# Kernel tuning notes

Measured on AMD Instinct MI355X. Metric: run time of the kernel, lower is better.

## Reference

```python
import jax, jax.numpy as jnp
import numpy as np

N_NODES = 100_000
E_OFF = 1_000_000
HID = 32
GF = 8
NF = 8
N_LAYERS = 3


def _mlp(h, W1, b1, W2, b2):
    # Linear -> ReLU -> Linear (matches MLP([in, hidden, out]))
    return jax.nn.relu(h @ W1 + b1) @ W2 + b2


def _seg_mean(v, idx, n):
    s = jax.ops.segment_sum(v, idx, num_segments=n)
    c = jax.ops.segment_sum(jnp.ones((v.shape[0], 1), v.dtype), idx, num_segments=n)
    return s / jnp.maximum(c, 1.0)


def _graphnet(x, row, col, eattr2, g, p):
    # GraphNet with global block: edge MLP -> mean-aggregate to nodes -> node MLP -> global MLP
    eW1, eb1, eW2, eb2, nW1, nb1, nW2, nb2, gW1, gb1, gW2, gb2 = p
    n, e = x.shape[0], row.shape[0]
    gE = jnp.broadcast_to(g, (e, g.shape[1]))
    e_emb = _mlp(jnp.concatenate([gE, x[row], x[col], eattr2], axis=1), eW1, eb1, eW2, eb2)
    agg = _seg_mean(e_emb, row, n)
    gN = jnp.broadcast_to(g, (n, g.shape[1]))
    n_emb = _mlp(jnp.concatenate([gN, x, agg], axis=1), nW1, nb1, nW2, nb2)
    g_new = _mlp(jnp.concatenate([n_emb.mean(0, keepdims=True), e_emb.mean(0, keepdims=True), g], axis=1),
                 gW1, gb1, gW2, gb2)
    return e_emb, n_emb, g_new


def setup_inputs() -> dict:
    key = jax.random.key(0)
    ks = jax.random.split(key, 24)
    a = jax.random.randint(ks[0], (E_OFF,), 0, N_NODES)
    b = jax.random.randint(ks[1], (E_OFF,), 0, N_NODES)
    d = jnp.arange(N_NODES)
    l_ei = jnp.stack([jnp.concatenate([jnp.maximum(a, b), d]),
                      jnp.concatenate([jnp.minimum(a, b), d])])  # lower triangular + diag
    c = jax.random.randint(ks[2], (E_OFF,), 0, N_NODES)
    e = jax.random.randint(ks[3], (E_OFF,), 0, N_NODES)
    u_ei = jnp.stack([jnp.concatenate([jnp.minimum(c, e), d]),
                      jnp.concatenate([jnp.maximum(c, e), d])])  # upper triangular + diag
    E = E_OFF + N_NODES
    x = jax.random.normal(ks[4], (N_NODES, NF), dtype=jnp.float32)
    l_attr = jax.random.normal(ks[5], (E, 1), dtype=jnp.float32)
    u_attr = jax.random.normal(ks[6], (E, 1), dtype=jnp.float32)

    def w(k, shape):
        return (jax.random.normal(k, shape, dtype=jnp.float32) / np.sqrt(shape[-2])).astype(jnp.float32)

    e_in = GF + 2 * NF + 1 + 1  # 26 (edge attr padded to 2: skip col, zeros where absent)
    n_in = GF + 1 + NF          # 17
    g_in = NF + 1 + GF          # 17
    return {
        'x': x, 'l_edge_index': l_ei, 'u_edge_index': u_ei,
        'l_edge_attr': l_attr, 'u_edge_attr': u_attr,
        'eW1': w(ks[7], (2, N_LAYERS, e_in, HID)), 'eb1': 0.01 * jax.random.normal(ks[8], (2, N_LAYERS, HID)),
        'eW2': w(ks[9], (2, N_LAYERS, HID, 1)), 'eb2': 0.01 * jax.random.normal(ks[10], (2, N_LAYERS, 1)),
        'nW1': w(ks[11], (2, N_LAYERS, n_in, HID)), 'nb1': 0.01 * jax.random.normal(ks[12], (2, N_LAYERS, HID)),
        'nW2': w(ks[13], (2, N_LAYERS, HID, NF)), 'nb2': 0.01 * jax.random.normal(ks[14], (2, N_LAYERS, NF)),
        'gW1': w(ks[15], (2, N_LAYERS, g_in, HID)), 'gb1': 0.01 * jax.random.normal(ks[16], (2, N_LAYERS, HID)),
        'gW2': w(ks[17], (2, N_LAYERS, HID, GF)), 'gb2': 0.01 * jax.random.normal(ks[18], (2, N_LAYERS, GF)),
    }


def reference(x, l_edge_index, u_edge_index, l_edge_attr, u_edge_attr,
              eW1, eb1, eW2, eb2, nW1, nb1, nW2, nb2, gW1, gb1, gW2, gb2):
    params = (eW1, eb1, eW2, eb2, nW1, nb1, nW2, nb2, gW1, gb1, gW2, gb2)
    lr, lc = l_edge_index[0], l_edge_index[1]
    ur, uc = u_edge_index[0], u_edge_index[1]
    g = jnp.zeros((1, GF), x.dtype)
    l_e, u_e = l_edge_attr, u_edge_attr
    l_a = l_edge_attr  # skip-connection edge features (original matrix values)
    zl, zu = jnp.zeros_like(l_edge_attr), jnp.zeros_like(u_edge_attr)
    for i in range(N_LAYERS):
        p1 = tuple(w[0, i] for w in params)
        p2 = tuple(w[1, i] for w in params)
        l_in = jnp.concatenate([l_e, l_a if i != 0 else zl], axis=1)  # zeros col == no skip (block 0)
        l_e, l_n, g = _graphnet(x, lr, lc, l_in, g, p1)
        u_in = jnp.concatenate([u_e, zu], axis=1)  # l2 never has skip; padded zeros col
        u_e, u_n, g = _graphnet(l_n, ur, uc, u_in, g, p2)
        # NOTE: node embeddings are NOT carried across MP blocks in the original
    l_vals = jnp.where(lr == lc, jnp.exp(l_e[:, 0]), l_e[:, 0])
    u_vals = jnp.where(ur == uc, jnp.exp(u_e[:, 0]), u_e[:, 0])
    return jnp.concatenate([l_vals, u_vals])
```

## Files before the change

### kernel.cpp

```cpp
#include <hip/hip_runtime.h>


typedef unsigned int u32;

#define NB_SHIFT 9
#define NB_SIZE 512
#define RSTRIDE 1104

__device__ __forceinline__ float wave_sum(float v) {
#pragma unroll
    for (int off = 32; off > 0; off >>= 1) v += __shfl_down(v, off, 64);
    return v;
}


__global__ __launch_bounds__(256) void hist_kernel(
    const int* __restrict__ lr, const int* __restrict__ ur,
    u32* __restrict__ hist, int E, int B) {
    __shared__ u32 h[256];
    const int t = threadIdx.x;
    if (t < B) h[t] = 0;
    __syncthreads();
    const int s = blockIdx.y;
    const int* rows = s ? ur : lr;
    for (int i = blockIdx.x * 256 + t; i < E; i += gridDim.x * 256)
        atomicAdd(&h[rows[i] >> NB_SHIFT], 1u);
    __syncthreads();
    if (t < B && h[t]) atomicAdd(&hist[s * B + t], h[t]);
}

__global__ void scan_kernel(const u32* __restrict__ hist, u32* __restrict__ offs,
                            u32* __restrict__ cur, int B) {
    if (threadIdx.x == 0) {
        for (int s = 0; s < 2; ++s) {
            u32 acc = 0;
            for (int b = 0; b < B; ++b) {
                offs[s * (B + 1) + b] = acc;
                cur[s * B + b] = acc;
                acc += hist[s * B + b];
            }
            offs[s * (B + 1) + B] = acc;
        }
    }
}

#define SCHUNK 4096
__global__ __launch_bounds__(256) void scatter_kernel(
    const int* __restrict__ lr, const int* __restrict__ ur,
    u32* __restrict__ cur, u32* __restrict__ list, int E, int B) {
    __shared__ u32 lcnt[256], lbase[256];
    const int t = threadIdx.x;
    const int s = blockIdx.y;
    const int* rows = s ? ur : lr;
    u32* mylist = list + (size_t)s * E;
    if (t < B) lcnt[t] = 0;
    __syncthreads();
    const int base_e = blockIdx.x * SCHUNK;
#pragma unroll
    for (int k = 0; k < SCHUNK / 256; ++k) {
        const int e = base_e + k * 256 + t;
        if (e < E) atomicAdd(&lcnt[rows[e] >> NB_SHIFT], 1u);
    }
    __syncthreads();
    if (t < B) {
        const u32 c = lcnt[t];
        lbase[t] = c ? atomicAdd(&cur[s * B + t], c) : 0u;
        lcnt[t] = 0;
    }
    __syncthreads();
#pragma unroll
    for (int k = 0; k < SCHUNK / 256; ++k) {
        const int e = base_e + k * 256 + t;
        if (e < E) {
            const int b = rows[e] >> NB_SHIFT;
            const u32 pos = lbase[b] + atomicAdd(&lcnt[b], 1u);
            mylist[pos] = (u32)e;
        }
    }
}


template <bool COUNT>
__global__ __launch_bounds__(1024) void agg_kernel(
    const u32* __restrict__ list, const u32* __restrict__ offs,
    const int* __restrict__ rows, const float* __restrict__ e_emb,
    float* __restrict__ agg, float* __restrict__ cntf, int N) {
    __shared__ float sbin[NB_SIZE];
    __shared__ float cbin[NB_SIZE];
    const int t = threadIdx.x;
    const int b = blockIdx.x;
    if (t < NB_SIZE) {
        sbin[t] = 0.0f;
        if constexpr (COUNT) cbin[t] = 0.0f;
    }
    __syncthreads();
    const u32 beg = offs[b], end = offs[b + 1];
    for (u32 i = beg + t; i < end; i += 1024) {
        const u32 eid = list[i];
        const float v = e_emb[eid];
        const int r = rows[eid];
        atomicAdd(&sbin[r & (NB_SIZE - 1)], v);
        if constexpr (COUNT) atomicAdd(&cbin[r & (NB_SIZE - 1)], 1.0f);
    }
    __syncthreads();
    const int n0 = b << NB_SHIFT;
    if (t < NB_SIZE && n0 + t < N) {
        agg[n0 + t] = sbin[t];
        if constexpr (COUNT) cntf[n0 + t] = cbin[t];
    }
}


template <bool SKIP, bool GAGG, bool VALS, bool STORE>
__global__ __launch_bounds__(256) void edge_kernel(
    const float4* __restrict__ xf,
    const int* __restrict__ rows, const int* __restrict__ cols,
    const float* __restrict__ eprev,
    const float* __restrict__ skipattr,
    const float* __restrict__ W1,
    const float* __restrict__ b1,
    const float* __restrict__ W2,
    const float* __restrict__ b2,
    const float* __restrict__ gbuf,
    float* __restrict__ e_out,
    float* __restrict__ vals_out,
    float* __restrict__ ebins,
    int E) {
    __shared__ float biasE[32];
    __shared__ float wpart[4];
    const int t = threadIdx.x;
    if (t < 32) {
        float v = b1[t];
#pragma unroll
        for (int k = 0; k < 8; ++k) v = fmaf(gbuf[k], W1[k * 32 + t], v);
        biasE[t] = v;
    }
    __syncthreads();
    const int e = blockIdx.x * 256 + t;
    const bool valid = e < E;
    const int idx = valid ? e : 0;
    const int r = rows[idx];
    const int c = cols[idx];
    const float4 xr0 = xf[2 * r], xr1 = xf[2 * r + 1];
    const float4 xc0 = xf[2 * c], xc1 = xf[2 * c + 1];
    float in[18] = {xr0.x, xr0.y, xr0.z, xr0.w, xr1.x, xr1.y, xr1.z, xr1.w,
                    xc0.x, xc0.y, xc0.z, xc0.w, xc1.x, xc1.y, xc1.z, xc1.w,
                    eprev[idx], 0.0f};
    if constexpr (SKIP) in[17] = skipattr[idx];
    float h[32];
#pragma unroll
    for (int j = 0; j < 8; ++j) {
        const float4 b = reinterpret_cast<const float4*>(biasE)[j];
        h[4 * j + 0] = b.x; h[4 * j + 1] = b.y;
        h[4 * j + 2] = b.z; h[4 * j + 3] = b.w;
    }
    const float* __restrict__ Wk = W1 + 8 * 32;
#pragma unroll
    for (int k = 0; k < 18; ++k) {
        const float v = in[k];
#pragma unroll
        for (int j = 0; j < 32; ++j) h[j] = fmaf(v, Wk[k * 32 + j], h[j]);
    }
    float out = b2[0];
#pragma unroll
    for (int j = 0; j < 32; ++j) out = fmaf(fmaxf(h[j], 0.0f), W2[j], out);

    if (valid) {
        if constexpr (STORE) e_out[e] = out;
        if constexpr (VALS) vals_out[e] = (r == c) ? expf(out) : out;
    }
    if constexpr (GAGG) {
        const float s = wave_sum(valid ? out : 0.0f);
        if ((t & 63) == 0) wpart[t >> 6] = s;
        __syncthreads();
        if (t == 0)
            atomicAdd(&ebins[blockIdx.x & 63],
                      wpart[0] + wpart[1] + wpart[2] + wpart[3]);
    }
}


template <bool STORE_N>
__global__ __launch_bounds__(256) void node_kernel(
    const float4* __restrict__ xf,
    const float* __restrict__ agg_sum, const float* __restrict__ cntf,
    const float* __restrict__ gbuf,
    const float* __restrict__ nW1, const float* __restrict__ nb1,
    const float* __restrict__ nW2, const float* __restrict__ nb2,
    float* __restrict__ n_out,
    float* __restrict__ nbins,
    int N) {
    __shared__ float biasN[32];
    __shared__ float npart[4][8];
    const int t = threadIdx.x;
    if (t < 32) {
        float v = nb1[t];
#pragma unroll
        for (int k = 0; k < 8; ++k) v = fmaf(gbuf[k], nW1[k * 32 + t], v);
        biasN[t] = v;
    }
    __syncthreads();
    const int n = blockIdx.x * 256 + t;
    const bool valid = n < N;
    const int idx = valid ? n : 0;
    const float4 x0 = xf[2 * idx], x1 = xf[2 * idx + 1];
    const float agg = agg_sum[idx] / fmaxf(cntf[idx], 1.0f);
    float in[9] = {x0.x, x0.y, x0.z, x0.w, x1.x, x1.y, x1.z, x1.w, agg};
    float h[32];
#pragma unroll
    for (int j = 0; j < 8; ++j) {
        const float4 b = reinterpret_cast<const float4*>(biasN)[j];
        h[4 * j + 0] = b.x; h[4 * j + 1] = b.y;
        h[4 * j + 2] = b.z; h[4 * j + 3] = b.w;
    }
    const float* __restrict__ Wk = nW1 + 8 * 32;
#pragma unroll
    for (int k = 0; k < 9; ++k) {
        const float v = in[k];
#pragma unroll
        for (int j = 0; j < 32; ++j) h[j] = fmaf(v, Wk[k * 32 + j], h[j]);
    }
    float o[8];
#pragma unroll
    for (int q = 0; q < 8; ++q) o[q] = nb2[q];
#pragma unroll
    for (int j = 0; j < 32; ++j) {
        const float hv = fmaxf(h[j], 0.0f);
#pragma unroll
        for (int q = 0; q < 8; ++q) o[q] = fmaf(hv, nW2[j * 8 + q], o[q]);
    }
    if constexpr (STORE_N) {
        if (valid) {
            reinterpret_cast<float4*>(n_out)[2 * n] =
                make_float4(o[0], o[1], o[2], o[3]);
            reinterpret_cast<float4*>(n_out)[2 * n + 1] =
                make_float4(o[4], o[5], o[6], o[7]);
        }
    }
#pragma unroll
    for (int q = 0; q < 8; ++q) {
        const float s = wave_sum(valid ? o[q] : 0.0f);
        if ((t & 63) == 0) npart[t >> 6][q] = s;
    }
    __syncthreads();
    if (t < 8)
        atomicAdd(&nbins[(blockIdx.x & 63) * 16 + t],
                  npart[0][t] + npart[1][t] + npart[2][t] + npart[3][t]);
}


__global__ __launch_bounds__(64) void global_kernel(
    const float* __restrict__ ebins,
    const float* __restrict__ nbins,
    const float* __restrict__ gW1, const float* __restrict__ gb1,
    const float* __restrict__ gW2, const float* __restrict__ gb2,
    float* __restrict__ gbuf,
    int N, float inv_E) {
    const int t = threadIdx.x;
    float nb[8];
#pragma unroll
    for (int q = 0; q < 8; ++q) nb[q] = nbins[t * 16 + q];
    const float eb = ebins[t];
    float gin[17];
#pragma unroll
    for (int q = 0; q < 8; ++q) {
        const float s = wave_sum(nb[q]);
        gin[q] = __shfl(s, 0, 64) / (float)N;
    }
    const float es = wave_sum(eb);
    gin[8] = __shfl(es, 0, 64) * inv_E;
#pragma unroll
    for (int k = 0; k < 8; ++k) gin[9 + k] = gbuf[k];
    float hv = 0.0f;
    if (t < 32) {
        hv = gb1[t];
#pragma unroll
        for (int k = 0; k < 17; ++k) hv = fmaf(gin[k], gW1[k * 32 + t], hv);
        hv = fmaxf(hv, 0.0f);
    }
#pragma unroll
    for (int q = 0; q < 8; ++q) {
        const float c = (t < 32) ? hv * gW2[t * 8 + q] : 0.0f;
        const float s = wave_sum(c);
        if (t == 0) gbuf[q] = gb2[q] + s;
    }
}

extern "C" void kernel_launch(void* const* d_in, const int* in_sizes, int n_in,
                              void* d_out, int out_size, void* d_ws,
                              size_t ws_size, hipStream_t stream) {
    const float* x = (const float*)d_in[0];
    const int* l_ei = (const int*)d_in[1];
    const int* u_ei = (const int*)d_in[2];
    const float* l_attr = (const float*)d_in[3];
    const float* u_attr = (const float*)d_in[4];
    const float* eW1 = (const float*)d_in[5];
    const float* eb1 = (const float*)d_in[6];
    const float* eW2 = (const float*)d_in[7];
    const float* eb2 = (const float*)d_in[8];
    const float* nW1 = (const float*)d_in[9];
    const float* nb1 = (const float*)d_in[10];
    const float* nW2 = (const float*)d_in[11];
    const float* nb2 = (const float*)d_in[12];
    const float* gW1 = (const float*)d_in[13];
    const float* gb1 = (const float*)d_in[14];
    const float* gW2 = (const float*)d_in[15];
    const float* gb2 = (const float*)d_in[16];

    const int E = in_sizes[3];
    const int N = in_sizes[0] / 8;
    const int B = (N + NB_SIZE - 1) >> NB_SHIFT;

    float* ws = (float*)d_ws;
    float* l_e = ws;
    float* u_e = l_e + E;
    float* l_n = u_e + E;
    float* agg = l_n + (size_t)8 * N;
    float* cnt_l = agg + N;
    float* cnt_u = cnt_l + N;
    float* gbuf = cnt_u + N;
    u32* hist = (u32*)(gbuf + 8);
    float* dyn_all = (float*)(hist + 2 * B);
    u32* offs = (u32*)(dyn_all + 5 * RSTRIDE);
    u32* cur = offs + 2 * (B + 1);
    u32* list = cur + 2 * B;

    const int* lr = l_ei;
    const int* lc = l_ei + E;
    const int* ur = u_ei;
    const int* uc = u_ei + E;
    const int eg = (E + 255) / 256;
    const int ng = (N + 255) / 256;
    const int sg = (E + SCHUNK - 1) / SCHUNK;
    const float invE = 1.0f / (float)E;
    float* outL = (float*)d_out;
    float* outU = outL + E;
    const u32* offs_l = offs;
    const u32* offs_u = offs + (B + 1);
    const u32* list_l = list;
    const u32* list_u = list + E;

    hipMemsetAsync(gbuf, 0, (size_t)(8 + 2 * B + 5 * RSTRIDE) * sizeof(float),
                   stream);
    hist_kernel<<<dim3(128, 2), 256, 0, stream>>>(lr, ur, hist, E, B);
    scan_kernel<<<1, 64, 0, stream>>>(hist, offs, cur, B);
    scatter_kernel<<<dim3(sg, 2), 256, 0, stream>>>(lr, ur, cur, list, E, B);

    int reg = 0;
    for (int i = 0; i < 3; ++i) {
        const size_t lo = (size_t)i;
        const size_t up = (size_t)(3 + i);

        float* ebins = dyn_all + (size_t)reg * RSTRIDE;
        float* nbins = ebins + 64;
        ++reg;
        const float* eprev = (i == 0) ? l_attr : l_e;
        if (i == 0)
            edge_kernel<false, true, false, true><<<eg, 256, 0, stream>>>(
                (const float4*)x, lr, lc, eprev, l_attr, eW1 + lo * 832,
                eb1 + lo * 32, eW2 + lo * 32, eb2 + lo, gbuf, l_e, outL, ebins, E);
        else if (i == 1)
            edge_kernel<true, true, false, true><<<eg, 256, 0, stream>>>(
                (const float4*)x, lr, lc, eprev, l_attr, eW1 + lo * 832,
                eb1 + lo * 32, eW2 + lo * 32, eb2 + lo, gbuf, l_e, outL, ebins, E);
        else
            edge_kernel<true, true, true, true><<<eg, 256, 0, stream>>>(
                (const float4*)x, lr, lc, eprev, l_attr, eW1 + lo * 832,
                eb1 + lo * 32, eW2 + lo * 32, eb2 + lo, gbuf, l_e, outL, ebins, E);
        if (i == 0)
            agg_kernel<true><<<B, 1024, 0, stream>>>(list_l, offs_l, lr, l_e,
                                                     agg, cnt_l, N);
        else
            agg_kernel<false><<<B, 1024, 0, stream>>>(list_l, offs_l, lr, l_e,
                                                      agg, cnt_l, N);
        node_kernel<true><<<ng, 256, 0, stream>>>(
            (const float4*)x, agg, cnt_l, gbuf, nW1 + lo * 544, nb1 + lo * 32,
            nW2 + lo * 256, nb2 + lo * 8, l_n, nbins, N);
        global_kernel<<<1, 64, 0, stream>>>(ebins, nbins, gW1 + lo * 544,
                                            gb1 + lo * 32, gW2 + lo * 256,
                                            gb2 + lo * 8, gbuf, N, invE);

        if (i < 2) {
            float* ebins2 = dyn_all + (size_t)reg * RSTRIDE;
            float* nbins2 = ebins2 + 64;
            ++reg;
            const float* ueprev = (i == 0) ? u_attr : u_e;
            edge_kernel<false, true, false, true><<<eg, 256, 0, stream>>>(
                (const float4*)l_n, ur, uc, ueprev, nullptr, eW1 + up * 832,
                eb1 + up * 32, eW2 + up * 32, eb2 + up, gbuf, u_e, nullptr,
                ebins2, E);
            if (i == 0)
                agg_kernel<true><<<B, 1024, 0, stream>>>(list_u, offs_u, ur,
                                                         u_e, agg, cnt_u, N);
            else
                agg_kernel<false><<<B, 1024, 0, stream>>>(list_u, offs_u, ur,
                                                          u_e, agg, cnt_u, N);
            node_kernel<false><<<ng, 256, 0, stream>>>(
                (const float4*)l_n, agg, cnt_u, gbuf, nW1 + up * 544,
                nb1 + up * 32, nW2 + up * 256, nb2 + up * 8, nullptr, nbins2,
                N);
            global_kernel<<<1, 64, 0, stream>>>(ebins2, nbins2, gW1 + up * 544,
                                                gb1 + up * 32, gW2 + up * 256,
                                                gb2 + up * 8, gbuf, N, invE);
        } else {
            edge_kernel<false, false, true, false><<<eg, 256, 0, stream>>>(
                (const float4*)l_n, ur, uc, u_e, nullptr, eW1 + up * 832,
                eb1 + up * 32, eW2 + up * 32, eb2 + up, gbuf, nullptr, outU,
                ebins, E);
        }
    }
}
```

Baseline: 570.0 us.

## Fuse global MLP into edge kernel and aggregation into node kernel

Removes the separate single-block global_kernel by having every edge-kernel block recompute the global MLP from the previous stage's bins, with block 0 writing the result to a per-stage slot. It also fuses segment aggregation with the node MLP so each 512-node bucket is reduced in shared memory and consumed directly, dropping the agg buffer round trip. The edge kernel becomes a grid-stride loop over a fixed 1024-block grid. Together this cuts kernel launches and serialization bubbles, at the cost of redundant per-block global-MLP work and only half the threads of the 1024-thread node blocks doing MLP work.

```diff
diff --git a/kernel.cpp b/kernel.cpp
--- a/kernel.cpp
+++ b/kernel.cpp
@@ -6,6 +6,7 @@
 #define NB_SHIFT 9
 #define NB_SIZE 512
 #define RSTRIDE 1104
+#define EG_BLOCKS 1024
 
 __device__ __forceinline__ float wave_sum(float v) {
 #pragma unroll
@@ -80,38 +81,7 @@
 }
 
 
-template <bool COUNT>
-__global__ __launch_bounds__(1024) void agg_kernel(
-    const u32* __restrict__ list, const u32* __restrict__ offs,
-    const int* __restrict__ rows, const float* __restrict__ e_emb,
-    float* __restrict__ agg, float* __restrict__ cntf, int N) {
-    __shared__ float sbin[NB_SIZE];
-    __shared__ float cbin[NB_SIZE];
-    const int t = threadIdx.x;
-    const int b = blockIdx.x;
-    if (t < NB_SIZE) {
-        sbin[t] = 0.0f;
-        if constexpr (COUNT) cbin[t] = 0.0f;
-    }
-    __syncthreads();
-    const u32 beg = offs[b], end = offs[b + 1];
-    for (u32 i = beg + t; i < end; i += 1024) {
-        const u32 eid = list[i];
-        const float v = e_emb[eid];
-        const int r = rows[eid];
-        atomicAdd(&sbin[r & (NB_SIZE - 1)], v);
-        if constexpr (COUNT) atomicAdd(&cbin[r & (NB_SIZE - 1)], 1.0f);
-    }
-    __syncthreads();
-    const int n0 = b << NB_SHIFT;
-    if (t < NB_SIZE && n0 + t < N) {
-        agg[n0 + t] = sbin[t];
-        if constexpr (COUNT) cntf[n0 + t] = cbin[t];
-    }
-}
-
-
-template <bool SKIP, bool GAGG, bool VALS, bool STORE>
+template <bool SKIP, bool GAGG, bool VALS, bool STORE, bool GCOMP>
 __global__ __launch_bounds__(256) void edge_kernel(
     const float4* __restrict__ xf,
     const int* __restrict__ rows, const int* __restrict__ cols,
@@ -121,56 +91,102 @@
     const float* __restrict__ b1,
     const float* __restrict__ W2,
     const float* __restrict__ b2,
-    const float* __restrict__ gbuf,
+    const float* __restrict__ gprev,
+    float* __restrict__ gout,
+    const float* __restrict__ pebins,
+    const float* __restrict__ pnbins,
+    const float* __restrict__ gW1, const float* __restrict__ gb1,
+    const float* __restrict__ gW2, const float* __restrict__ gb2,
+    float* __restrict__ ebins,
     float* __restrict__ e_out,
     float* __restrict__ vals_out,
-    float* __restrict__ ebins,
-    int E) {
+    int E, int N, float inv_E) {
+    __shared__ float gsh[8];
     __shared__ float biasE[32];
     __shared__ float wpart[4];
     const int t = threadIdx.x;
+    if constexpr (GCOMP) {
+        if (t < 64) {
+            float nb[8];
+#pragma unroll
+            for (int q = 0; q < 8; ++q) nb[q] = pnbins[t * 16 + q];
+            const float eb = pebins[t];
+            float gin[17];
+#pragma unroll
+            for (int q = 0; q < 8; ++q) {
+                const float s = wave_sum(nb[q]);
+                gin[q] = __shfl(s, 0, 64) / (float)N;
+            }
+            const float es = wave_sum(eb);
+            gin[8] = __shfl(es, 0, 64) * inv_E;
+#pragma unroll
+            for (int k = 0; k < 8; ++k) gin[9 + k] = gprev[k];
+            float hv = 0.0f;
+            if (t < 32) {
+                hv = gb1[t];
+#pragma unroll
+                for (int k = 0; k < 17; ++k)
+                    hv = fmaf(gin[k], gW1[k * 32 + t], hv);
+                hv = fmaxf(hv, 0.0f);
+            }
+#pragma unroll
+            for (int q = 0; q < 8; ++q) {
+                const float c = (t < 32) ? hv * gW2[t * 8 + q] : 0.0f;
+                const float s = wave_sum(c);
+                if (t == 0) {
+                    const float gv = gb2[q] + s;
+                    gsh[q] = gv;
+                    if (blockIdx.x == 0) gout[q] = gv;
+                }
+            }
+        }
+    } else {
+        if (t < 8) gsh[t] = gprev[t];
+    }
+    __syncthreads();
     if (t < 32) {
         float v = b1[t];
 #pragma unroll
-        for (int k = 0; k < 8; ++k) v = fmaf(gbuf[k], W1[k * 32 + t], v);
+        for (int k = 0; k < 8; ++k) v = fmaf(gsh[k], W1[k * 32 + t], v);
         biasE[t] = v;
     }
     __syncthreads();
-    const int e = blockIdx.x * 256 + t;
-    const bool valid = e < E;
-    const int idx = valid ? e : 0;
-    const int r = rows[idx];
-    const int c = cols[idx];
-    const float4 xr0 = xf[2 * r], xr1 = xf[2 * r + 1];
-    const float4 xc0 = xf[2 * c], xc1 = xf[2 * c + 1];
-    float in[18] = {xr0.x, xr0.y, xr0.z, xr0.w, xr1.x, xr1.y, xr1.z, xr1.w,
-                    xc0.x, xc0.y, xc0.z, xc0.w, xc1.x, xc1.y, xc1.z, xc1.w,
-                    eprev[idx], 0.0f};
-    if constexpr (SKIP) in[17] = skipattr[idx];
-    float h[32];
-#pragma unroll
-    for (int j = 0; j < 8; ++j) {
-        const float4 b = reinterpret_cast<const float4*>(biasE)[j];
-        h[4 * j + 0] = b.x; h[4 * j + 1] = b.y;
-        h[4 * j + 2] = b.z; h[4 * j + 3] = b.w;
-    }
+
     const float* __restrict__ Wk = W1 + 8 * 32;
-#pragma unroll
-    for (int k = 0; k < 18; ++k) {
-        const float v = in[k];
-#pragma unroll
-        for (int j = 0; j < 32; ++j) h[j] = fmaf(v, Wk[k * 32 + j], h[j]);
-    }
-    float out = b2[0];
-#pragma unroll
-    for (int j = 0; j < 32; ++j) out = fmaf(fmaxf(h[j], 0.0f), W2[j], out);
-
-    if (valid) {
+    float accsum = 0.0f;
+    const int stride = gridDim.x * 256;
+    for (int e = blockIdx.x * 256 + t; e < E; e += stride) {
+        const int r = rows[e];
+        const int c = cols[e];
+        const float4 xr0 = xf[2 * r], xr1 = xf[2 * r + 1];
+        const float4 xc0 = xf[2 * c], xc1 = xf[2 * c + 1];
+        float in[18] = {xr0.x, xr0.y, xr0.z, xr0.w, xr1.x, xr1.y, xr1.z,
+                        xr1.w, xc0.x, xc0.y, xc0.z, xc0.w, xc1.x, xc1.y,
+                        xc1.z, xc1.w, eprev[e], 0.0f};
+        if constexpr (SKIP) in[17] = skipattr[e];
+        float h[32];
+#pragma unroll
+        for (int j = 0; j < 8; ++j) {
+            const float4 b = reinterpret_cast<const float4*>(biasE)[j];
+            h[4 * j + 0] = b.x; h[4 * j + 1] = b.y;
+            h[4 * j + 2] = b.z; h[4 * j + 3] = b.w;
+        }
+#pragma unroll
+        for (int k = 0; k < 18; ++k) {
+            const float v = in[k];
+#pragma unroll
+            for (int j = 0; j < 32; ++j) h[j] = fmaf(v, Wk[k * 32 + j], h[j]);
+        }
+        float out = b2[0];
+#pragma unroll
+        for (int j = 0; j < 32; ++j) out = fmaf(fmaxf(h[j], 0.0f), W2[j], out);
+
         if constexpr (STORE) e_out[e] = out;
         if constexpr (VALS) vals_out[e] = (r == c) ? expf(out) : out;
+        if constexpr (GAGG) accsum += out;
     }
     if constexpr (GAGG) {
-        const float s = wave_sum(valid ? out : 0.0f);
+        const float s = wave_sum(accsum);
         if ((t & 63) == 0) wpart[t >> 6] = s;
         __syncthreads();
         if (t == 0)
@@ -180,109 +196,104 @@
 }
 
 
-template <bool STORE_N>
-__global__ __launch_bounds__(256) void node_kernel(
+template <bool COUNT, bool STORE_N>
+__global__ __launch_bounds__(1024) void aggnode_kernel(
+    const u32* __restrict__ list, const u32* __restrict__ offs,
+    const int* __restrict__ rows, const float* __restrict__ e_emb,
     const float4* __restrict__ xf,
-    const float* __restrict__ agg_sum, const float* __restrict__ cntf,
-    const float* __restrict__ gbuf,
+    float* __restrict__ cntf,
+    const float* __restrict__ g,
     const float* __restrict__ nW1, const float* __restrict__ nb1,
     const float* __restrict__ nW2, const float* __restrict__ nb2,
     float* __restrict__ n_out,
     float* __restrict__ nbins,
     int N) {
+    __shared__ float sbin[NB_SIZE];
+    __shared__ float cbin[NB_SIZE];
     __shared__ float biasN[32];
-    __shared__ float npart[4][8];
+    __shared__ float npart[8][8];
     const int t = threadIdx.x;
-    if (t < 32) {
-        float v = nb1[t];
-#pragma unroll
-        for (int k = 0; k < 8; ++k) v = fmaf(gbuf[k], nW1[k * 32 + t], v);
-        biasN[t] = v;
-    }
-    __syncthreads();
-    const int n = blockIdx.x * 256 + t;
-    const bool valid = n < N;
-    const int idx = valid ? n : 0;
-    const float4 x0 = xf[2 * idx], x1 = xf[2 * idx + 1];
-    const float agg = agg_sum[idx] / fmaxf(cntf[idx], 1.0f);
-    float in[9] = {x0.x, x0.y, x0.z, x0.w, x1.x, x1.y, x1.z, x1.w, agg};
-    float h[32];
-#pragma unroll
-    for (int j = 0; j < 8; ++j) {
-        const float4 b = reinterpret_cast<const float4*>(biasN)[j];
-        h[4 * j + 0] = b.x; h[4 * j + 1] = b.y;
-        h[4 * j + 2] = b.z; h[4 * j + 3] = b.w;
-    }
-    const float* __restrict__ Wk = nW1 + 8 * 32;
-#pragma unroll
-    for (int k = 0; k < 9; ++k) {
-        const float v = in[k];
-#pragma unroll
-        for (int j = 0; j < 32; ++j) h[j] = fmaf(v, Wk[k * 32 + j], h[j]);
-    }
+    if (t < NB_SIZE) {
+        sbin[t] = 0.0f;
+        if constexpr (COUNT) cbin[t] = 0.0f;
+    }
+    if (t >= NB_SIZE && t < NB_SIZE + 32) {
+        const int j = t - NB_SIZE;
+        float v = nb1[j];
+#pragma unroll
+        for (int k = 0; k < 8; ++k) v = fmaf(g[k], nW1[k * 32 + j], v);
+        biasN[j] = v;
+    }
+    __syncthreads();
+    const int b = blockIdx.x;
+    const u32 beg = offs[b], end = offs[b + 1];
+    for (u32 i = beg + t; i < end; i += 1024) {
+        const u32 eid = list[i];
+        const float v = e_emb[eid];
+        const int r = rows[eid];
+        atomicAdd(&sbin[r & (NB_SIZE - 1)], v);
+        if constexpr (COUNT) atomicAdd(&cbin[r & (NB_SIZE - 1)], 1.0f);
+    }
+    __syncthreads();
+
+    const int n0 = b << NB_SHIFT;
     float o[8];
-#pragma unroll
-    for (int q = 0; q < 8; ++q) o[q] = nb2[q];
-#pragma unroll
-    for (int j = 0; j < 32; ++j) {
-        const float hv = fmaxf(h[j], 0.0f);
-#pragma unroll
-        for (int q = 0; q < 8; ++q) o[q] = fmaf(hv, nW2[j * 8 + q], o[q]);
-    }
-    if constexpr (STORE_N) {
-        if (valid) {
-            reinterpret_cast<float4*>(n_out)[2 * n] =
-                make_float4(o[0], o[1], o[2], o[3]);
-            reinterpret_cast<float4*>(n_out)[2 * n + 1] =
-                make_float4(o[4], o[5], o[6], o[7]);
-        }
-    }
-#pragma unroll
-    for (int q = 0; q < 8; ++q) {
-        const float s = wave_sum(valid ? o[q] : 0.0f);
-        if ((t & 63) == 0) npart[t >> 6][q] = s;
-    }
-    __syncthreads();
-    if (t < 8)
-        atomicAdd(&nbins[(blockIdx.x & 63) * 16 + t],
-                  npart[0][t] + npart[1][t] + npart[2][t] + npart[3][t]);
-}
-
-
-__global__ __launch_bounds__(64) void global_kernel(
-    const float* __restrict__ ebins,
-    const float* __restrict__ nbins,
-    const float* __restrict__ gW1, const float* __restrict__ gb1,
-    const float* __restrict__ gW2, const float* __restrict__ gb2,
-    float* __restrict__ gbuf,
-    int N, float inv_E) {
-    const int t = threadIdx.x;
-    float nb[8];
-#pragma unroll
-    for (int q = 0; q < 8; ++q) nb[q] = nbins[t * 16 + q];
-    const float eb = ebins[t];
-    float gin[17];
-#pragma unroll
-    for (int q = 0; q < 8; ++q) {
-        const float s = wave_sum(nb[q]);
-        gin[q] = __shfl(s, 0, 64) / (float)N;
-    }
-    const float es = wave_sum(eb);
-    gin[8] = __shfl(es, 0, 64) * inv_E;
-#pragma unroll
-    for (int k = 0; k < 8; ++k) gin[9 + k] = gbuf[k];
-    float hv = 0.0f;
-    if (t < 32) {
-        hv = gb1[t];
-#pragma unroll
-        for (int k = 0; k < 17; ++k) hv = fmaf(gin[k], gW1[k * 32 + t], hv);
-        hv = fmaxf(hv, 0.0f);
-    }
-#pragma unroll
-    for (int q = 0; q < 8; ++q) {
-        const float c = (t < 32) ? hv * gW2[t * 8 + q] : 0.0f;
-        const float s = wave_sum(c);
-        if (t == 0) gbuf[q] = gb2[q] + s;
+    const bool active = (t < NB_SIZE) && (n0 + t < N);
+    if (t < NB_SIZE) {
+        const int n = n0 + t;
+        const int idx = active ? n : (N - 1);
+        float cntv;
+        if constexpr (COUNT) {
+            cntv = cbin[t];
+            if (active) cntf[n] = cntv;
+        } else {
+            cntv = cntf[idx];
+        }
+        const float agg = sbin[t] / fmaxf(cntv, 1.0f);
+        const float4 x0 = xf[2 * idx], x1 = xf[2 * idx + 1];
+        float in[9] = {x0.x, x0.y, x0.z, x0.w, x1.x, x1.y, x1.z, x1.w, agg};
+        float h[32];
+#pragma unroll
+        for (int j = 0; j < 8; ++j) {
+            const float4 bb = reinterpret_cast<const float4*>(biasN)[j];
+            h[4 * j + 0] = bb.x; h[4 * j + 1] = bb.y;
+            h[4 * j + 2] = bb.z; h[4 * j + 3] = bb.w;
+        }
+        const float* __restrict__ Wk = nW1 + 8 * 32;
+#pragma unroll
+        for (int k = 0; k < 9; ++k) {
+            const float v = in[k];
+#pragma unroll
+            for (int j = 0; j < 32; ++j) h[j] = fmaf(v, Wk[k * 32 + j], h[j]);
+        }
+#pragma unroll
+        for (int q = 0; q < 8; ++q) o[q] = nb2[q];
+#pragma unroll
+        for (int j = 0; j < 32; ++j) {
+            const float hv = fmaxf(h[j], 0.0f);
+#pragma unroll
+            for (int q = 0; q < 8; ++q) o[q] = fmaf(hv, nW2[j * 8 + q], o[q]);
+        }
+        if constexpr (STORE_N) {
+            if (active) {
+                reinterpret_cast<float4*>(n_out)[2 * n] =
+                    make_float4(o[0], o[1], o[2], o[3]);
+                reinterpret_cast<float4*>(n_out)[2 * n + 1] =
+                    make_float4(o[4], o[5], o[6], o[7]);
+            }
+        }
+#pragma unroll
+        for (int q = 0; q < 8; ++q) {
+            const float s = wave_sum(active ? o[q] : 0.0f);
+            if ((t & 63) == 0) npart[t >> 6][q] = s;
+        }
+    }
+    __syncthreads();
+    if (t < 8) {
+        float a = 0.0f;
+#pragma unroll
+        for (int w = 0; w < 8; ++w) a += npart[w][t];
+        atomicAdd(&nbins[(b & 63) * 16 + t], a);
     }
 }
 
@@ -315,11 +326,10 @@
     float* l_e = ws;
     float* u_e = l_e + E;
     float* l_n = u_e + E;
-    float* agg = l_n + (size_t)8 * N;
-    float* cnt_l = agg + N;
+    float* cnt_l = l_n + (size_t)8 * N;
     float* cnt_u = cnt_l + N;
-    float* gbuf = cnt_u + N;
-    u32* hist = (u32*)(gbuf + 8);
+    float* gslot = cnt_u + N;
+    u32* hist = (u32*)(gslot + 56);
     float* dyn_all = (float*)(hist + 2 * B);
     u32* offs = (u32*)(dyn_all + 5 * RSTRIDE);
     u32* cur = offs + 2 * (B + 1);
@@ -329,8 +339,6 @@
     const int* lc = l_ei + E;
     const int* ur = u_ei;
     const int* uc = u_ei + E;
-    const int eg = (E + 255) / 256;
-    const int ng = (N + 255) / 256;
     const int sg = (E + SCHUNK - 1) / SCHUNK;
     const float invE = 1.0f / (float)E;
     float* outL = (float*)d_out;
@@ -340,73 +348,78 @@
     const u32* list_l = list;
     const u32* list_u = list + E;
 
-    hipMemsetAsync(gbuf, 0, (size_t)(8 + 2 * B + 5 * RSTRIDE) * sizeof(float),
+    hipMemsetAsync(gslot, 0, (size_t)(56 + 2 * B + 5 * RSTRIDE) * sizeof(float),
                    stream);
     hist_kernel<<<dim3(128, 2), 256, 0, stream>>>(lr, ur, hist, E, B);
     scan_kernel<<<1, 64, 0, stream>>>(hist, offs, cur, B);
     scatter_kernel<<<dim3(sg, 2), 256, 0, stream>>>(lr, ur, cur, list, E, B);
 
-    int reg = 0;
-    for (int i = 0; i < 3; ++i) {
-        const size_t lo = (size_t)i;
-        const size_t up = (size_t)(3 + i);
-
-        float* ebins = dyn_all + (size_t)reg * RSTRIDE;
+    const size_t wsl[6] = {0, 3, 1, 4, 2, 5};
+
+    for (int j = 0; j < 6; ++j) {
+        const bool lower = !(j & 1);
+        const size_t sl = wsl[j];
+        float* ebins = dyn_all + (size_t)(j <= 4 ? j : 4) * RSTRIDE;
         float* nbins = ebins + 64;
-        ++reg;
-        const float* eprev = (i == 0) ? l_attr : l_e;
-        if (i == 0)
-            edge_kernel<false, true, false, true><<<eg, 256, 0, stream>>>(
-                (const float4*)x, lr, lc, eprev, l_attr, eW1 + lo * 832,
-                eb1 + lo * 32, eW2 + lo * 32, eb2 + lo, gbuf, l_e, outL, ebins, E);
-        else if (i == 1)
-            edge_kernel<true, true, false, true><<<eg, 256, 0, stream>>>(
-                (const float4*)x, lr, lc, eprev, l_attr, eW1 + lo * 832,
-                eb1 + lo * 32, eW2 + lo * 32, eb2 + lo, gbuf, l_e, outL, ebins, E);
-        else
-            edge_kernel<true, true, true, true><<<eg, 256, 0, stream>>>(
-                (const float4*)x, lr, lc, eprev, l_attr, eW1 + lo * 832,
-                eb1 + lo * 32, eW2 + lo * 32, eb2 + lo, gbuf, l_e, outL, ebins, E);
-        if (i == 0)
-            agg_kernel<true><<<B, 1024, 0, stream>>>(list_l, offs_l, lr, l_e,
-                                                     agg, cnt_l, N);
-        else
-            agg_kernel<false><<<B, 1024, 0, stream>>>(list_l, offs_l, lr, l_e,
-                                                      agg, cnt_l, N);
-        node_kernel<true><<<ng, 256, 0, stream>>>(
-            (const float4*)x, agg, cnt_l, gbuf, nW1 + lo * 544, nb1 + lo * 32,
-            nW2 + lo * 256, nb2 + lo * 8, l_n, nbins, N);
-        global_kernel<<<1, 64, 0, stream>>>(ebins, nbins, gW1 + lo * 544,
-                                            gb1 + lo * 32, gW2 + lo * 256,
-                                            gb2 + lo * 8, gbuf, N, invE);
-
-        if (i < 2) {
-            float* ebins2 = dyn_all + (size_t)reg * RSTRIDE;
-            float* nbins2 = ebins2 + 64;
-            ++reg;
-            const float* ueprev = (i == 0) ? u_attr : u_e;
-            edge_kernel<false, true, false, true><<<eg, 256, 0, stream>>>(
-                (const float4*)l_n, ur, uc, ueprev, nullptr, eW1 + up * 832,
-                eb1 + up * 32, eW2 + up * 32, eb2 + up, gbuf, u_e, nullptr,
-                ebins2, E);
-            if (i == 0)
-                agg_kernel<true><<<B, 1024, 0, stream>>>(list_u, offs_u, ur,
-                                                         u_e, agg, cnt_u, N);
-            else
-                agg_kernel<false><<<B, 1024, 0, stream>>>(list_u, offs_u, ur,
-                                                          u_e, agg, cnt_u, N);
-            node_kernel<false><<<ng, 256, 0, stream>>>(
-                (const float4*)l_n, agg, cnt_u, gbuf, nW1 + up * 544,
-                nb1 + up * 32, nW2 + up * 256, nb2 + up * 8, nullptr, nbins2,
-                N);
-            global_kernel<<<1, 64, 0, stream>>>(ebins2, nbins2, gW1 + up * 544,
-                                                gb1 + up * 32, gW2 + up * 256,
-                                                gb2 + up * 8, gbuf, N, invE);
-        } else {
-            edge_kernel<false, false, true, false><<<eg, 256, 0, stream>>>(
-                (const float4*)l_n, ur, uc, u_e, nullptr, eW1 + up * 832,
-                eb1 + up * 32, eW2 + up * 32, eb2 + up, gbuf, nullptr, outU,
-                ebins, E);
-        }
-    }
-}
+        const float* pe = (j >= 1) ? dyn_all + (size_t)(j - 1) * RSTRIDE : nullptr;
+        const float* pn = (j >= 1) ? pe + 64 : nullptr;
+        const size_t psl = (j >= 1) ? wsl[j - 1] : 0;
+        const float4* exf = (const float4*)(lower ? x : l_n);
+        const int* rows = lower ? lr : ur;
+        const int* cols = lower ? lc : uc;
+        const float* eprev = (j == 0) ? l_attr
+                             : (j == 1) ? u_attr
+                             : (lower ? l_e : u_e);
+        float* e_out = lower ? l_e : u_e;
+        const float* gprev = gslot + (size_t)(j >= 1 ? j - 1 : 0) * 8;
+        float* gout = gslot + (size_t)j * 8;
+
+#define EDGE_ARGS                                                             \
+    exf, rows, cols, eprev, l_attr, eW1 + sl * 832, eb1 + sl * 32,            \
+        eW2 + sl * 32, eb2 + sl, gprev, gout, pe, pn, gW1 + psl * 544,        \
+        gb1 + psl * 32, gW2 + psl * 256, gb2 + psl * 8, ebins,                \
+        e_out, (j == 4) ? outL : outU, E, N, invE
+
+        switch (j) {
+            case 0: edge_kernel<false, true, false, true, false>
+                        <<<EG_BLOCKS, 256, 0, stream>>>(EDGE_ARGS); break;
+            case 1: edge_kernel<false, true, false, true, true>
+                        <<<EG_BLOCKS, 256, 0, stream>>>(EDGE_ARGS); break;
+            case 2: edge_kernel<true, true, false, true, true>
+                        <<<EG_BLOCKS, 256, 0, stream>>>(EDGE_ARGS); break;
+            case 3: edge_kernel<false, true, false, true, true>
+                        <<<EG_BLOCKS, 256, 0, stream>>>(EDGE_ARGS); break;
+            case 4: edge_kernel<true, true, true, true, true>
+                        <<<EG_BLOCKS, 256, 0, stream>>>(EDGE_ARGS); break;
+            case 5: edge_kernel<false, false, true, false, true>
+                        <<<EG_BLOCKS, 256, 0, stream>>>(EDGE_ARGS); break;
+        }
+#undef EDGE_ARGS
+
+        if (j == 5) break;
+
+        const u32* alist = lower ? list_l : list_u;
+        const u32* aoffs = lower ? offs_l : offs_u;
+        float* cntf = lower ? cnt_l : cnt_u;
+        const float4* nxf = (const float4*)(lower ? x : l_n);
+
+#define AGG_ARGS                                                              \
+    alist, aoffs, rows, e_out, nxf, cntf, gslot + (size_t)j * 8,              \
+        nW1 + sl * 544, nb1 + sl * 32, nW2 + sl * 256, nb2 + sl * 8, l_n,     \
+        nbins, N
+
+        switch (j) {
+            case 0: aggnode_kernel<true, true>
+                        <<<B, 1024, 0, stream>>>(AGG_ARGS); break;
+            case 1: aggnode_kernel<true, false>
+                        <<<B, 1024, 0, stream>>>(AGG_ARGS); break;
+            case 2: aggnode_kernel<false, true>
+                        <<<B, 1024, 0, stream>>>(AGG_ARGS); break;
+            case 3: aggnode_kernel<false, false>
+                        <<<B, 1024, 0, stream>>>(AGG_ARGS); break;
+            case 4: aggnode_kernel<false, true>
+                        <<<B, 1024, 0, stream>>>(AGG_ARGS); break;
+        }
+#undef AGG_ARGS
+    }
+}
```

Result: slower. 649.2 us (+13.9%).
